# Kernel optimization log

Hardware: AMD Instinct MI355X
Metric: run time of the kernel (lower is better)

## Reference

```python
import jax, jax.numpy as jnp
import numpy as np

N_NODES = 100000
N_EDGES = 1600000
NODE_DIM = 128
HIDDEN = 128
OUT_DIM = 128
N_GRAPHS = 64
LN_EPS = 1e-5


def setup_inputs() -> dict:
    key = jax.random.key(0)
    ks = jax.random.split(key, 14)

    def lin(k, fan_in, fan_out):
        bound = 1.0 / np.sqrt(fan_in)
        kw, kb = jax.random.split(k)
        W = jax.random.uniform(kw, (fan_in, fan_out), jnp.float32, -bound, bound)
        b = jax.random.uniform(kb, (fan_out,), jnp.float32, -bound, bound)
        return W, b

    node_features = jax.random.normal(ks[0], (N_NODES, NODE_DIM), jnp.float32)
    edge_index = jax.random.randint(ks[1], (2, N_EDGES), 0, N_NODES, jnp.int32)
    batch = jnp.sort(jax.random.randint(ks[2], (N_NODES,), 0, N_GRAPHS, jnp.int32))

    W1, b1 = lin(ks[3], NODE_DIM, HIDDEN)
    W2, b2 = lin(ks[4], HIDDEN, HIDDEN)
    W3, b3 = lin(ks[5], HIDDEN, OUT_DIM)
    Wm1, bm1 = lin(ks[6], OUT_DIM, HIDDEN)
    Wm2, bm2 = lin(ks[7], HIDDEN, OUT_DIM)
    ln_g = jnp.ones((OUT_DIM,), jnp.float32)
    ln_b = jnp.zeros((OUT_DIM,), jnp.float32)

    return dict(node_features=node_features, edge_index=edge_index, batch=batch,
                W1=W1, b1=b1, W2=W2, b2=b2, W3=W3, b3=b3,
                Wm1=Wm1, bm1=bm1, Wm2=Wm2, bm2=bm2, ln_g=ln_g, ln_b=ln_b)


def _gcn_precompute(edge_index, n_nodes):
    # Add self-loops; symmetric degree normalization (PyG GCNConv semantics).
    loops = jnp.arange(n_nodes, dtype=edge_index.dtype)
    src = jnp.concatenate([edge_index[0], loops])
    dst = jnp.concatenate([edge_index[1], loops])
    deg = jax.ops.segment_sum(jnp.ones_like(dst, jnp.float32), dst, num_segments=n_nodes)
    dinv = jax.lax.rsqrt(deg)  # deg >= 1 thanks to self-loops
    norm = dinv[src] * dinv[dst]  # [E + N]
    return src, dst, norm


def _gcn_layer(x, W, b, src, dst, norm, n_nodes):
    xw = x @ W                              # [N, F_out]
    msg = norm[:, None] * xw[src]           # [E+N, F_out] gather
    agg = jax.ops.segment_sum(msg, dst, num_segments=n_nodes)  # scatter-add
    return agg + b


def reference(node_features, edge_index, batch,
              W1, b1, W2, b2, W3, b3, Wm1, bm1, Wm2, bm2, ln_g, ln_b):
    n_nodes = node_features.shape[0]
    src, dst, norm = _gcn_precompute(edge_index, n_nodes)

    x = jax.nn.relu(_gcn_layer(node_features, W1, b1, src, dst, norm, n_nodes))
    x = jax.nn.relu(_gcn_layer(x, W2, b2, src, dst, norm, n_nodes))
    x = _gcn_layer(x, W3, b3, src, dst, norm, n_nodes)  # no relu on last layer

    # global mean pool per graph
    sums = jax.ops.segment_sum(x, batch, num_segments=N_GRAPHS)
    cnts = jax.ops.segment_sum(jnp.ones((n_nodes,), x.dtype), batch, num_segments=N_GRAPHS)
    g = sums / jnp.maximum(cnts, 1.0)[:, None]  # [G, OUT_DIM]

    # global reasoner MLP + LayerNorm
    h = jax.nn.relu(g @ Wm1 + bm1)
    y = h @ Wm2 + bm2
    mu = jnp.mean(y, axis=-1, keepdims=True)
    var = jnp.var(y, axis=-1, keepdims=True)
    y = (y - mu) * jax.lax.rsqrt(var + LN_EPS) * ln_g + ln_b
    return y
```

## Files before the change

kernel.cpp:

```cpp
#include <hip/hip_runtime.h>

#define FDIM 128
#define LN_EPS 1e-5f
#define NBKT_SHIFT 10
#define BKT_NODES 1024
#define MAXBKT 128
#define CAP_SHIFT 15
#define BKT_CAP 32768

typedef short bf16x8 __attribute__((ext_vector_type(8)));
typedef float f32x4 __attribute__((ext_vector_type(4)));
typedef float f32x2 __attribute__((ext_vector_type(2)));
typedef ushort u16x8 __attribute__((ext_vector_type(8)));
typedef unsigned long long u64;
typedef long long i64;

static __device__ __forceinline__ ushort f2bf(float f) {
    union { float f; unsigned u; } v; v.f = f;
    unsigned r = v.u + 0x7FFFu + ((v.u >> 16) & 1u);
    return (ushort)(r >> 16);
}
static __device__ __forceinline__ float bf2f(ushort h) {
    union { unsigned u; float f; } v; v.u = ((unsigned)h) << 16;
    return v.f;
}
static __device__ __forceinline__ unsigned char f2fp8(float f) {
    return (unsigned char)__builtin_amdgcn_cvt_pk_fp8_f32(f, f, 0u, false);
}
static __device__ __forceinline__ float fp8tof(unsigned char b) {
    f32x2 p = __builtin_amdgcn_cvt_pk_f32_fp8((unsigned)b, false);
    return p[0];
}
static __device__ __forceinline__ void fp8x8_add(uint2 w, f32x2* acc) {
    acc[0] += __builtin_amdgcn_cvt_pk_f32_fp8(w.x, false);
    acc[1] += __builtin_amdgcn_cvt_pk_f32_fp8(w.x, true);
    acc[2] += __builtin_amdgcn_cvt_pk_f32_fp8(w.y, false);
    acc[3] += __builtin_amdgcn_cvt_pk_f32_fp8(w.y, true);
}


__launch_bounds__(256)
__global__ void k_bkt_scatter(const int* __restrict__ src, const int* __restrict__ dst,
                              int* __restrict__ bcur, unsigned* __restrict__ bktA,
                              int E, int nbkt) {
    __shared__ int h[2][MAXBKT], lbase[2][MAXBKT], lcur[2][MAXBKT];
    const int t = threadIdx.x;
    const int half = t >> 7;
    for (int i = t; i < 2 * MAXBKT; i += 256) ((int*)h)[i] = 0;
    __syncthreads();
    const int E4 = E >> 2;
    const int4* s4p = (const int4*)src;
    const int4* d4p = (const int4*)dst;
    int4 sv[4], dv[4]; bool ok[4];
#pragma unroll
    for (int r = 0; r < 4; r++) {
        int i4 = blockIdx.x * 1024 + r * 256 + t;
        ok[r] = (i4 < E4);
        if (ok[r]) {
            sv[r] = s4p[i4]; dv[r] = d4p[i4];
            atomicAdd(&h[half][dv[r].x >> NBKT_SHIFT], 1);
            atomicAdd(&h[half][dv[r].y >> NBKT_SHIFT], 1);
            atomicAdd(&h[half][dv[r].z >> NBKT_SHIFT], 1);
            atomicAdd(&h[half][dv[r].w >> NBKT_SHIFT], 1);
        }
    }
    __syncthreads();
    for (int i = t; i < 2 * nbkt; i += 256) {
        const int hh = (i >= nbkt) ? 1 : 0;
        const int b = hh ? (i - nbkt) : i;
        const int c = h[hh][b];
        lbase[hh][b] = c ? ((b << CAP_SHIFT) + atomicAdd(&bcur[b], c)) : 0;
        lcur[hh][b] = 0;
    }
    __syncthreads();
#pragma unroll
    for (int r = 0; r < 4; r++) {
        if (!ok[r]) continue;
        int ss[4] = {sv[r].x, sv[r].y, sv[r].z, sv[r].w};
        int dd[4] = {dv[r].x, dv[r].y, dv[r].z, dv[r].w};
#pragma unroll
        for (int j = 0; j < 4; j++) {
            int b = dd[j] >> NBKT_SHIFT;
            int p = atomicAdd(&lcur[half][b], 1);
            bktA[(size_t)lbase[half][b] + p] =
                ((unsigned)ss[j] << NBKT_SHIFT) | (unsigned)(dd[j] & (BKT_NODES - 1));
        }
    }
}


__launch_bounds__(1024)
__global__ void k_build(const unsigned* __restrict__ bktA, const int* __restrict__ bcur,
                        int2* __restrict__ rowinfo, float* __restrict__ dinv,
                        int* __restrict__ csr_src, int N) {
    __shared__ int cnt[BKT_NODES];
    __shared__ int cur[BKT_NODES];
    __shared__ int wpart[16], wbase[16];
    const int t = threadIdx.x;
    const int b = blockIdx.x;
    const int nb = b << NBKT_SHIFT;
    cnt[t] = 0;
    __syncthreads();
    const int beg = b << CAP_SHIFT;
    const int end = beg + bcur[b];
    for (int i = beg + t; i < end; i += 1024)
        atomicAdd(&cnt[bktA[i] & (BKT_NODES - 1)], 1);
    __syncthreads();
    const int lane = t & 63, wv = t >> 6;
    const int my = cnt[t];
    int x = my;
#pragma unroll
    for (int off = 1; off < 64; off <<= 1) {
        int y = __shfl_up(x, off, 64);
        if (lane >= off) x += y;
    }
    if (lane == 63) wpart[wv] = x;
    __syncthreads();
    if (t == 0) {
        int s = 0;
        for (int w = 0; w < 16; w++) { int tmp = wpart[w]; wbase[w] = s; s += tmp; }
    }
    __syncthreads();
    const int incl = x + wbase[wv];
    const int rbeg = beg + incl - my;
    cur[t] = rbeg;
    const int n = nb + t;
    if (n < N) {
        rowinfo[n] = make_int2(rbeg, my);
        dinv[n] = rsqrtf((float)(my + 1));
    }
    __syncthreads();
    for (int i = beg + t; i < end; i += 1024) {
        unsigned pr = bktA[i];
        int d = pr & (BKT_NODES - 1);
        int p = atomicAdd(&cur[d], 1);
        csr_src[p] = (int)(pr >> NBKT_SHIFT);
    }
}


__global__ void k_prep_w(const float* __restrict__ Wa, const float* __restrict__ Wb,
                         const float* __restrict__ Wc, ushort* __restrict__ Wt_b,
                         unsigned char* __restrict__ Wt8, float* __restrict__ gsums,
                         int* __restrict__ bcur) {
    int idx = blockIdx.x * 256 + threadIdx.x;
    int layer = idx >> 14;
    int r = idx & 16383;
    int nn = r >> 7, kk = r & 127;
    if (layer == 0) {
        Wt_b[r] = f2bf(Wa[kk * 128 + nn]);
    } else {
        const float* W = (layer == 1) ? Wb : Wc;
        Wt8[(size_t)(layer - 1) * 16384 + r] = f2fp8(W[kk * 128 + nn]);
    }
    if (idx < 8192) gsums[idx] = 0.f;
    if (idx < MAXBKT) bcur[idx] = 0;
}


__launch_bounds__(256)
__global__ void k_gemm_f32(const float* __restrict__ X, const ushort* __restrict__ Wt,
                           const float* __restrict__ dinv, unsigned char* __restrict__ C,
                           int N) {
    __shared__ __align__(16) ushort As[128][136];
    __shared__ ushort Ws[128][136];
    const int t = threadIdx.x;
    const int row0 = blockIdx.x * 128;

#pragma unroll
    for (int i = 0; i < 8; i++) {
        int c = t + i * 256;
        int r = c >> 4, c8 = (c & 15) * 8;
        *(bf16x8*)&Ws[r][c8] = *(const bf16x8*)&Wt[r * 128 + c8];
    }
#pragma unroll
    for (int i = 0; i < 8; i++) {
        int c = t + i * 256;
        int r = c >> 4, c8 = (c & 15) * 8;
        int row = row0 + r;
        bf16x8 pk = {0, 0, 0, 0, 0, 0, 0, 0};
        if (row < N) {
            const float* sp = X + (size_t)row * FDIM + c8;
            float4 u0 = *(const float4*)(sp);
            float4 u1 = *(const float4*)(sp + 4);
            pk[0] = (short)f2bf(u0.x); pk[1] = (short)f2bf(u0.y);
            pk[2] = (short)f2bf(u0.z); pk[3] = (short)f2bf(u0.w);
            pk[4] = (short)f2bf(u1.x); pk[5] = (short)f2bf(u1.y);
            pk[6] = (short)f2bf(u1.z); pk[7] = (short)f2bf(u1.w);
        }
        *(bf16x8*)&As[r][c8] = pk;
    }
    __syncthreads();

    const int w = t >> 6, l = t & 63;
    const int m = l & 15, q = l >> 4;
    const int r0 = w * 32;

    bf16x8 a0[4], a1[4];
#pragma unroll
    for (int ks = 0; ks < 4; ks++) {
        a0[ks] = *(const bf16x8*)&As[r0 + m][ks * 32 + q * 8];
        a1[ks] = *(const bf16x8*)&As[r0 + 16 + m][ks * 32 + q * 8];
    }

    f32x4 acc0[8], acc1[8];
#pragma unroll
    for (int ct = 0; ct < 8; ct++) { acc0[ct] = {0, 0, 0, 0}; acc1[ct] = {0, 0, 0, 0}; }

#pragma unroll
    for (int ct = 0; ct < 8; ct++) {
#pragma unroll
        for (int ks = 0; ks < 4; ks++) {
            bf16x8 b = *(const bf16x8*)&Ws[ct * 16 + m][ks * 32 + q * 8];
            acc0[ct] = __builtin_amdgcn_mfma_f32_16x16x32_bf16(a0[ks], b, acc0[ct], 0, 0, 0);
            acc1[ct] = __builtin_amdgcn_mfma_f32_16x16x32_bf16(a1[ks], b, acc1[ct], 0, 0, 0);
        }
    }

    float dv0[4], dv1[4];
#pragma unroll
    for (int r = 0; r < 4; r++) {
        int row = row0 + r0 + q * 4 + r;
        dv0[r] = (row < N) ? dinv[row] : 0.f;
        dv1[r] = (row + 16 < N) ? dinv[row + 16] : 0.f;
    }

    __syncthreads();
    char* Ab = (char*)&As[0][0];
#pragma unroll
    for (int ct = 0; ct < 8; ct++) {
#pragma unroll
        for (int r = 0; r < 4; r++) {
            int rl = r0 + q * 4 + r;
            Ab[rl * 128 + ct * 16 + m] = (char)f2fp8(acc0[ct][r] * dv0[r]);
            Ab[(rl + 16) * 128 + ct * 16 + m] = (char)f2fp8(acc1[ct][r] * dv1[r]);
        }
    }
    __syncthreads();
    const uint4* As4 = (const uint4*)Ab;
#pragma unroll
    for (int i = 0; i < 4; i++) {
        int c = t + i * 256;
        int row = c >> 3;
        int col = (c & 7) * 16;
        int grow = row0 + row;
        if (grow < N) *(uint4*)&C[(size_t)grow * FDIM + col] = As4[c];
    }
}


__launch_bounds__(256)
__global__ void k_gemm_fp8(const unsigned char* __restrict__ X,
                           const unsigned char* __restrict__ W8,
                           const float* __restrict__ dinv, unsigned char* __restrict__ C,
                           int N) {
    __shared__ __align__(16) unsigned char As[128][144];
    __shared__ __align__(16) unsigned char Ws[128][144];
    const int t = threadIdx.x;
    const int row0 = blockIdx.x * 128;

#pragma unroll
    for (int i = 0; i < 4; i++) {
        int c = t + i * 256;
        int r = c >> 3, col = (c & 7) * 16;
        *(uint4*)&Ws[r][col] = *(const uint4*)&W8[r * 128 + col];
        int row = row0 + r;
        uint4 v = {0, 0, 0, 0};
        if (row < N) v = *(const uint4*)&X[(size_t)row * FDIM + col];
        *(uint4*)&As[r][col] = v;
    }
    __syncthreads();

    const int w = t >> 6, l = t & 63;
    const int m = l & 15, q = l >> 4;
    const int r0 = w * 32;

    i64 a0[4], a1[4];
#pragma unroll
    for (int ks = 0; ks < 4; ks++) {
        a0[ks] = *(const i64*)&As[r0 + m][ks * 32 + q * 8];
        a1[ks] = *(const i64*)&As[r0 + 16 + m][ks * 32 + q * 8];
    }

    f32x4 acc0[8], acc1[8];
#pragma unroll
    for (int ct = 0; ct < 8; ct++) { acc0[ct] = {0, 0, 0, 0}; acc1[ct] = {0, 0, 0, 0}; }

#pragma unroll
    for (int ct = 0; ct < 8; ct++) {
#pragma unroll
        for (int ks = 0; ks < 4; ks++) {
            i64 b = *(const i64*)&Ws[ct * 16 + m][ks * 32 + q * 8];
            acc0[ct] = __builtin_amdgcn_mfma_f32_16x16x32_fp8_fp8(a0[ks], b, acc0[ct], 0, 0, 0);
            acc1[ct] = __builtin_amdgcn_mfma_f32_16x16x32_fp8_fp8(a1[ks], b, acc1[ct], 0, 0, 0);
        }
    }

    float dv0[4], dv1[4];
#pragma unroll
    for (int r = 0; r < 4; r++) {
        int row = row0 + r0 + q * 4 + r;
        dv0[r] = (row < N) ? dinv[row] : 0.f;
        dv1[r] = (row + 16 < N) ? dinv[row + 16] : 0.f;
    }

    __syncthreads();
    char* Ab = (char*)&As[0][0];
#pragma unroll
    for (int ct = 0; ct < 8; ct++) {
#pragma unroll
        for (int r = 0; r < 4; r++) {
            int rl = r0 + q * 4 + r;
            Ab[rl * 128 + ct * 16 + m] = (char)f2fp8(acc0[ct][r] * dv0[r]);
            Ab[(rl + 16) * 128 + ct * 16 + m] = (char)f2fp8(acc1[ct][r] * dv1[r]);
        }
    }
    __syncthreads();
    const uint4* As4 = (const uint4*)Ab;
#pragma unroll
    for (int i = 0; i < 4; i++) {
        int c = t + i * 256;
        int row = c >> 3;
        int col = (c & 7) * 16;
        int grow = row0 + row;
        if (grow < N) *(uint4*)&C[(size_t)grow * FDIM + col] = As4[c];
    }
}


__launch_bounds__(256)
__global__ void k_aggregate(const unsigned char* __restrict__ xs8,
                            const int2* __restrict__ rowinfo,
                            const int* __restrict__ csr_src, const float* __restrict__ dinv,
                            const float* __restrict__ bias, unsigned char* __restrict__ out,
                            int N, int do_relu) {
    const int n = (blockIdx.x << 2) + (threadIdx.x >> 6);
    if (n >= N) return;
    const int l = threadIdx.x & 63;
    const int fl = l & 15;
    const int grp = l >> 4;

    const uint2* xsr = (const uint2*)xs8;

    f32x2 acc[4] = {{0, 0}, {0, 0}, {0, 0}, {0, 0}};
    if (grp == 0) {
        uint2 sv = xsr[(size_t)n * 16 + fl];
        fp8x8_add(sv, acc);
    }

    const int2 ri = rowinfo[n];
    const int beg = ri.x;
    const int deg = ri.y;

    for (int base = 0; base < deg; base += 64) {
        const int m = min(64, deg - base);
        int idx = 0;
        if (l < m) idx = csr_src[beg + base + l];
        int j = grp;
        if (j < m) {
            int s = __shfl(idx, j, 64);
            uint2 v = xsr[(size_t)s * 16 + fl];
#pragma unroll 2
            for (j += 4; j < m; j += 4) {
                int s2 = __shfl(idx, j, 64);
                uint2 v2 = xsr[(size_t)s2 * 16 + fl];
                fp8x8_add(v, acc);
                v = v2;
            }
            fp8x8_add(v, acc);
        }
    }

    float a[8] = {acc[0][0], acc[0][1], acc[1][0], acc[1][1],
                  acc[2][0], acc[2][1], acc[3][0], acc[3][1]};
#pragma unroll
    for (int k = 0; k < 8; k++) {
        a[k] += __shfl_xor(a[k], 16, 64);
        a[k] += __shfl_xor(a[k], 32, 64);
    }

    if (grp == 0) {
        const float d = dinv[n];
        const float4 b0 = ((const float4*)bias)[fl * 2];
        const float4 b1 = ((const float4*)bias)[fl * 2 + 1];
        const float bb[8] = {b0.x, b0.y, b0.z, b0.w, b1.x, b1.y, b1.z, b1.w};
        float v[8];
#pragma unroll
        for (int k = 0; k < 8; k++) {
            v[k] = d * a[k] + bb[k];
            if (do_relu) v[k] = fmaxf(v[k], 0.f);
        }
        uint2 o;
        unsigned d0 = __builtin_amdgcn_cvt_pk_fp8_f32(v[0], v[1], 0u, false);
        o.x = __builtin_amdgcn_cvt_pk_fp8_f32(v[2], v[3], d0, true);
        unsigned d1 = __builtin_amdgcn_cvt_pk_fp8_f32(v[4], v[5], 0u, false);
        o.y = __builtin_amdgcn_cvt_pk_fp8_f32(v[6], v[7], d1, true);
        ((uint2*)out)[(size_t)n * 16 + fl] = o;
    }
}


#define POOL_NODES 128

__launch_bounds__(128)
__global__ void k_pool(const unsigned char* __restrict__ x3, const int* __restrict__ batch,
                       float* __restrict__ sums, int N) {
    const int t = threadIdx.x;
    const int n0 = blockIdx.x * POOL_NODES;
    if (n0 >= N) return;
    const int n1 = (n0 + POOL_NODES < N) ? n0 + POOL_NODES : N;

    float acc = 0.f;
    int cur = batch[n0];
    for (int n = n0; n < n1; n++) {
        int g = batch[n];
        if (g != cur) {
            atomicAdd(&sums[cur * FDIM + t], acc);
            acc = 0.f;
            cur = g;
        }
        acc += fp8tof(x3[(size_t)n * FDIM + t]);
    }
    atomicAdd(&sums[cur * FDIM + t], acc);
}


__launch_bounds__(128)
__global__ void k_final(const float* __restrict__ sums, const int* __restrict__ batch, int N,
                        const float* __restrict__ Wm1, const float* __restrict__ bm1,
                        const float* __restrict__ Wm2, const float* __restrict__ bm2,
                        const float* __restrict__ ln_g, const float* __restrict__ ln_b,
                        float* __restrict__ out) {
    const int g = blockIdx.x;
    const int t = threadIdx.x;

    int lo = 0, hi = N;
    while (lo < hi) { int mid = (lo + hi) >> 1; if (batch[mid] < g) lo = mid + 1; else hi = mid; }
    int lo2 = lo, hi2 = N;
    while (lo2 < hi2) { int mid = (lo2 + hi2) >> 1; if (batch[mid] < g + 1) lo2 = mid + 1; else hi2 = mid; }
    float cnt = (float)(lo2 - lo);

    float gl = sums[g * FDIM + t] / fmaxf(cnt, 1.0f);

    __shared__ float gbuf[FDIM];
    __shared__ float hbuf[FDIM];
    __shared__ float wsum[4];
    gbuf[t] = gl;
    __syncthreads();

    float h = bm1[t];
#pragma unroll 8
    for (int k = 0; k < FDIM; k++) h += gbuf[k] * Wm1[k * FDIM + t];
    h = fmaxf(h, 0.f);
    hbuf[t] = h;
    __syncthreads();

    float y = bm2[t];
#pragma unroll 8
    for (int k = 0; k < FDIM; k++) y += hbuf[k] * Wm2[k * FDIM + t];

    float s = y, s2 = y * y;
#pragma unroll
    for (int off = 32; off > 0; off >>= 1) {
        s += __shfl_down(s, off, 64);
        s2 += __shfl_down(s2, off, 64);
    }
    if ((t & 63) == 0) { wsum[t >> 6] = s; wsum[2 + (t >> 6)] = s2; }
    __syncthreads();
    float sum = wsum[0] + wsum[1];
    float sumsq = wsum[2] + wsum[3];
    float mu = sum * (1.0f / FDIM);
    float var = sumsq * (1.0f / FDIM) - mu * mu;
    float r = rsqrtf(var + LN_EPS);
    out[g * FDIM + t] = (y - mu) * r * ln_g[t] + ln_b[t];
}


extern "C" void kernel_launch(void* const* d_in, const int* in_sizes, int n_in,
                              void* d_out, int out_size, void* d_ws, size_t ws_size,
                              hipStream_t stream) {
    const float* x_in  = (const float*)d_in[0];
    const int*   eidx  = (const int*)d_in[1];
    const int*   batch = (const int*)d_in[2];
    const float* W1 = (const float*)d_in[3];
    const float* b1 = (const float*)d_in[4];
    const float* W2 = (const float*)d_in[5];
    const float* b2 = (const float*)d_in[6];
    const float* W3 = (const float*)d_in[7];
    const float* b3 = (const float*)d_in[8];
    const float* Wm1 = (const float*)d_in[9];
    const float* bm1 = (const float*)d_in[10];
    const float* Wm2 = (const float*)d_in[11];
    const float* bm2 = (const float*)d_in[12];
    const float* ln_g = (const float*)d_in[13];
    const float* ln_b = (const float*)d_in[14];
    float* out = (float*)d_out;

    const int N = in_sizes[0] / FDIM;
    const int E = in_sizes[1] / 2;
    const int G = out_size / FDIM;

    const int* src = eidx;
    const int* dst = eidx + E;

    const int nbkt = (N + BKT_NODES - 1) >> NBKT_SHIFT;

    char* p = (char*)d_ws;
    unsigned* bktA = (unsigned*)p;    p += (size_t)nbkt * BKT_CAP * 4;
    unsigned char* B0q = (unsigned char*)p; p += (size_t)N * FDIM;
    unsigned char* B1q = (unsigned char*)p; p += (size_t)N * FDIM;
    int* csr_src = (int*)p;           p += (size_t)nbkt * BKT_CAP * 4;
    int2* rowinfo = (int2*)p;         p += (size_t)N * 8;
    float* dinv = (float*)p;          p += (size_t)N * 4;
    ushort* Wt_b = (ushort*)p;        p += 16384 * 2;
    unsigned char* Wt8 = (unsigned char*)p; p += 2 * 16384;
    float* gsums = (float*)p;         p += (size_t)G * FDIM * 4;
    int* bcur = (int*)p;              p += MAXBKT * 4;

    const int TPB = 256;
    dim3 blk(TPB);
    dim3 gAgg((N + 3) / 4);
    dim3 gTile((N + 127) / 128);
    const int nEb = (E + 4095) / 4096;

    k_prep_w<<<dim3(192), blk, 0, stream>>>(W1, W2, W3, Wt_b, Wt8, gsums, bcur);
    k_bkt_scatter<<<dim3(nEb), blk, 0, stream>>>(src, dst, bcur, bktA, E, nbkt);
    k_build<<<dim3(nbkt), dim3(1024), 0, stream>>>(bktA, bcur, rowinfo, dinv, csr_src, N);

    k_gemm_f32<<<gTile, blk, 0, stream>>>(x_in, Wt_b, dinv, B0q, N);
    k_aggregate<<<gAgg, blk, 0, stream>>>(B0q, rowinfo, csr_src, dinv, b1, B1q, N, 1);

    k_gemm_fp8<<<gTile, blk, 0, stream>>>(B1q, Wt8, dinv, B0q, N);
    k_aggregate<<<gAgg, blk, 0, stream>>>(B0q, rowinfo, csr_src, dinv, b2, B1q, N, 1);

    k_gemm_fp8<<<gTile, blk, 0, stream>>>(B1q, Wt8 + 16384, dinv, B0q, N);
    k_aggregate<<<gAgg, blk, 0, stream>>>(B0q, rowinfo, csr_src, dinv, b3, B1q, N, 0);

    k_pool<<<dim3((N + POOL_NODES - 1) / POOL_NODES), dim3(FDIM), 0, stream>>>(B1q, batch, gsums, N);
    k_final<<<dim3(G), dim3(FDIM), 0, stream>>>(gsums, batch, N, Wm1, bm1, Wm2, bm2,
                                                ln_g, ln_b, out);
}
```

Before: 425.9 us.

## Shrink buckets, sort CSR in LDS, deepen aggregate prefetch, vectorize pooling

Bucket size drops from 1024 to 256 nodes so there are more, smaller buckets. k_build now scatters edges into a shared-memory buffer and then writes csr_src in one coalesced pass instead of scattering to global memory. The aggregate kernel prefetches two neighbor rows ahead and uses 32-bit unsigned address math. Pooling reads four fp8 values per thread and uses more threads per block. The 8192-entry LDS buffer relies on a bucket never holding more than 8192 edges, which holds for uniform random edges but could overflow on skewed graphs.

```diff
diff --git a/kernel.cpp b/kernel.cpp
--- a/kernel.cpp
+++ b/kernel.cpp
@@ -2,11 +2,11 @@
 
 #define FDIM 128
 #define LN_EPS 1e-5f
-#define NBKT_SHIFT 10
-#define BKT_NODES 1024
-#define MAXBKT 128
-#define CAP_SHIFT 15
-#define BKT_CAP 32768
+#define NBKT_SHIFT 8
+#define BKT_NODES 256
+#define MAXBKT 512
+#define CAP_SHIFT 13
+#define BKT_CAP 8192
 
 typedef short bf16x8 __attribute__((ext_vector_type(8)));
 typedef float f32x4 __attribute__((ext_vector_type(4)));
@@ -89,53 +89,62 @@
 }
 
 
-__launch_bounds__(1024)
+__launch_bounds__(512)
 __global__ void k_build(const unsigned* __restrict__ bktA, const int* __restrict__ bcur,
                         int2* __restrict__ rowinfo, float* __restrict__ dinv,
                         int* __restrict__ csr_src, int N) {
+    __shared__ int sorted[BKT_CAP];
     __shared__ int cnt[BKT_NODES];
     __shared__ int cur[BKT_NODES];
-    __shared__ int wpart[16], wbase[16];
+    __shared__ int wpart[4], wbase[4];
     const int t = threadIdx.x;
     const int b = blockIdx.x;
     const int nb = b << NBKT_SHIFT;
-    cnt[t] = 0;
+    if (t < BKT_NODES) cnt[t] = 0;
     __syncthreads();
     const int beg = b << CAP_SHIFT;
-    const int end = beg + bcur[b];
-    for (int i = beg + t; i < end; i += 1024)
-        atomicAdd(&cnt[bktA[i] & (BKT_NODES - 1)], 1);
+    const int tot = bcur[b];
+    for (int i = t; i < tot; i += 512)
+        atomicAdd(&cnt[bktA[beg + i] & (BKT_NODES - 1)], 1);
     __syncthreads();
     const int lane = t & 63, wv = t >> 6;
-    const int my = cnt[t];
-    int x = my;
-#pragma unroll
-    for (int off = 1; off < 64; off <<= 1) {
-        int y = __shfl_up(x, off, 64);
-        if (lane >= off) x += y;
-    }
-    if (lane == 63) wpart[wv] = x;
+    int my = 0, x = 0;
+    if (t < BKT_NODES) {
+        my = cnt[t];
+        x = my;
+#pragma unroll
+        for (int off = 1; off < 64; off <<= 1) {
+            int y = __shfl_up(x, off, 64);
+            if (lane >= off) x += y;
+        }
+        if (lane == 63) wpart[wv] = x;
+    }
     __syncthreads();
     if (t == 0) {
         int s = 0;
-        for (int w = 0; w < 16; w++) { int tmp = wpart[w]; wbase[w] = s; s += tmp; }
-    }
-    __syncthreads();
-    const int incl = x + wbase[wv];
-    const int rbeg = beg + incl - my;
-    cur[t] = rbeg;
-    const int n = nb + t;
-    if (n < N) {
-        rowinfo[n] = make_int2(rbeg, my);
-        dinv[n] = rsqrtf((float)(my + 1));
-    }
-    __syncthreads();
-    for (int i = beg + t; i < end; i += 1024) {
-        unsigned pr = bktA[i];
+        for (int w = 0; w < 4; w++) { int tmp = wpart[w]; wbase[w] = s; s += tmp; }
+    }
+    __syncthreads();
+    if (t < BKT_NODES) {
+        const int incl = x + wbase[wv];
+        const int rbeg = incl - my;
+        cur[t] = rbeg;
+        const int n = nb + t;
+        if (n < N) {
+            rowinfo[n] = make_int2(beg + rbeg, my);
+            dinv[n] = rsqrtf((float)(my + 1));
+        }
+    }
+    __syncthreads();
+    for (int i = t; i < tot; i += 512) {
+        unsigned pr = bktA[beg + i];
         int d = pr & (BKT_NODES - 1);
         int p = atomicAdd(&cur[d], 1);
-        csr_src[p] = (int)(pr >> NBKT_SHIFT);
-    }
+        sorted[p] = (int)(pr >> NBKT_SHIFT);
+    }
+    __syncthreads();
+    for (int i = t; i < tot; i += 512)
+        csr_src[beg + i] = sorted[i];
 }
 
 
@@ -339,12 +348,11 @@
     const int l = threadIdx.x & 63;
     const int fl = l & 15;
     const int grp = l >> 4;
-
-    const uint2* xsr = (const uint2*)xs8;
+    const unsigned foff = (unsigned)fl << 3;
 
     f32x2 acc[4] = {{0, 0}, {0, 0}, {0, 0}, {0, 0}};
     if (grp == 0) {
-        uint2 sv = xsr[(size_t)n * 16 + fl];
+        uint2 sv = *(const uint2*)(xs8 + (((unsigned)n << 7) | foff));
         fp8x8_add(sv, acc);
     }
 
@@ -355,19 +363,26 @@
     for (int base = 0; base < deg; base += 64) {
         const int m = min(64, deg - base);
         int idx = 0;
-        if (l < m) idx = csr_src[beg + base + l];
+        if (l < m) idx = csr_src[(unsigned)(beg + base + l)];
         int j = grp;
         if (j < m) {
-            int s = __shfl(idx, j, 64);
-            uint2 v = xsr[(size_t)s * 16 + fl];
-#pragma unroll 2
-            for (j += 4; j < m; j += 4) {
-                int s2 = __shfl(idx, j, 64);
-                uint2 v2 = xsr[(size_t)s2 * 16 + fl];
-                fp8x8_add(v, acc);
-                v = v2;
+            int s0 = __shfl(idx, j, 64);
+            uint2 v0 = *(const uint2*)(xs8 + (((unsigned)s0 << 7) | foff));
+            int j2 = j + 4;
+            if (j2 < m) {
+                int s1 = __shfl(idx, j2, 64);
+                uint2 v1 = *(const uint2*)(xs8 + (((unsigned)s1 << 7) | foff));
+                for (j = j2 + 4; j < m; j += 4) {
+                    int s2 = __shfl(idx, j, 64);
+                    uint2 v2 = *(const uint2*)(xs8 + (((unsigned)s2 << 7) | foff));
+                    fp8x8_add(v0, acc);
+                    v0 = v1; v1 = v2;
+                }
+                fp8x8_add(v0, acc);
+                fp8x8_add(v1, acc);
+            } else {
+                fp8x8_add(v0, acc);
             }
-            fp8x8_add(v, acc);
         }
     }
 
@@ -400,28 +415,35 @@
 }
 
 
-#define POOL_NODES 128
-
-__launch_bounds__(128)
+__launch_bounds__(256)
 __global__ void k_pool(const unsigned char* __restrict__ x3, const int* __restrict__ batch,
                        float* __restrict__ sums, int N) {
     const int t = threadIdx.x;
-    const int n0 = blockIdx.x * POOL_NODES;
+    const int fq = t & 31;
+    const int sub = t >> 5;
+    const int n0 = blockIdx.x * 256 + sub * 32;
     if (n0 >= N) return;
-    const int n1 = (n0 + POOL_NODES < N) ? n0 + POOL_NODES : N;
-
-    float acc = 0.f;
+    const int n1 = (n0 + 32 < N) ? n0 + 32 : N;
+
+    f32x4 acc = {0.f, 0.f, 0.f, 0.f};
     int cur = batch[n0];
     for (int n = n0; n < n1; n++) {
         int g = batch[n];
         if (g != cur) {
-            atomicAdd(&sums[cur * FDIM + t], acc);
-            acc = 0.f;
+            float* s = &sums[cur * FDIM + (fq << 2)];
+            atomicAdd(s + 0, acc[0]); atomicAdd(s + 1, acc[1]);
+            atomicAdd(s + 2, acc[2]); atomicAdd(s + 3, acc[3]);
+            acc = (f32x4){0.f, 0.f, 0.f, 0.f};
             cur = g;
         }
-        acc += fp8tof(x3[(size_t)n * FDIM + t]);
-    }
-    atomicAdd(&sums[cur * FDIM + t], acc);
+        unsigned w = *(const unsigned*)(x3 + ((size_t)n << 7) + (fq << 2));
+        f32x2 lo = __builtin_amdgcn_cvt_pk_f32_fp8(w, false);
+        f32x2 hi = __builtin_amdgcn_cvt_pk_f32_fp8(w, true);
+        acc[0] += lo[0]; acc[1] += lo[1]; acc[2] += hi[0]; acc[3] += hi[1];
+    }
+    float* s = &sums[cur * FDIM + (fq << 2)];
+    atomicAdd(s + 0, acc[0]); atomicAdd(s + 1, acc[1]);
+    atomicAdd(s + 2, acc[2]); atomicAdd(s + 3, acc[3]);
 }
 
 
@@ -525,7 +547,7 @@
 
     k_prep_w<<<dim3(192), blk, 0, stream>>>(W1, W2, W3, Wt_b, Wt8, gsums, bcur);
     k_bkt_scatter<<<dim3(nEb), blk, 0, stream>>>(src, dst, bcur, bktA, E, nbkt);
-    k_build<<<dim3(nbkt), dim3(1024), 0, stream>>>(bktA, bcur, rowinfo, dinv, csr_src, N);
+    k_build<<<dim3(nbkt), dim3(512), 0, stream>>>(bktA, bcur, rowinfo, dinv, csr_src, N);
 
     k_gemm_f32<<<gTile, blk, 0, stream>>>(x_in, Wt_b, dinv, B0q, N);
     k_aggregate<<<gAgg, blk, 0, stream>>>(B0q, rowinfo, csr_src, dinv, b1, B1q, N, 1);
@@ -536,7 +558,7 @@
     k_gemm_fp8<<<gTile, blk, 0, stream>>>(B1q, Wt8 + 16384, dinv, B0q, N);
     k_aggregate<<<gAgg, blk, 0, stream>>>(B0q, rowinfo, csr_src, dinv, b3, B1q, N, 0);
 
-    k_pool<<<dim3((N + POOL_NODES - 1) / POOL_NODES), dim3(FDIM), 0, stream>>>(B1q, batch, gsums, N);
+    k_pool<<<dim3((N + 255) / 256), blk, 0, stream>>>(B1q, batch, gsums, N);
     k_final<<<dim3(G), dim3(FDIM), 0, stream>>>(gsums, batch, N, Wm1, bm1, Wm2, bm2,
                                                 ln_g, ln_b, out);
 }
```

Result: faster. 384.4 us (-9.8%).
